# Kernel optimization log

Measured on AMD Instinct MI355X. Metric: run time of the kernel, lower is better.

## Reference

```python
import jax, jax.numpy as jnp
from jax import lax
import numpy as np

K = 3          # kernel_size (must be 3 for shape consistency with the 3x3 sigma conv)
STRIDE = 2
C_IN = 128
EPS = 1e-5     # FrozenBatchNorm2d eps


def setup_inputs() -> dict:
    key = jax.random.key(0)
    k1, k2, k3, k4, k5, k6 = jax.random.split(key, 6)
    x = jax.random.normal(k1, (8, C_IN, 112, 112), dtype=jnp.float32)
    # conv: in_channels -> k*k, 3x3, no bias (kaiming init ~ normal scaled)
    fan_out = K * K * 3 * 3
    conv_w = jax.random.normal(k2, (K * K, C_IN, 3, 3), dtype=jnp.float32) * np.sqrt(2.0 / fan_out)
    bn_w = jax.random.normal(k3, (K * K,), dtype=jnp.float32) * 0.1 + 1.0
    bn_b = jax.random.normal(k4, (K * K,), dtype=jnp.float32) * 0.1
    bn_mean = jax.random.normal(k5, (K * K,), dtype=jnp.float32) * 0.1
    bn_var = jax.random.uniform(k6, (K * K,), dtype=jnp.float32, minval=0.5, maxval=1.5)
    return {"x": x, "conv_w": conv_w, "bn_w": bn_w, "bn_b": bn_b,
            "bn_mean": bn_mean, "bn_var": bn_var}


def _pasa(x, conv_w, bn_w, bn_b, bn_mean, bn_var):
    n, c, h, w = x.shape
    pad = K // 2
    # reflection pad
    xp = jnp.pad(x, ((0, 0), (0, 0), (pad, pad), (pad, pad)), mode="reflect")
    # 3x3 conv, stride 1, VALID on padded input -> same h, w
    sigma = lax.conv_general_dilated(xp, conv_w, (1, 1), "VALID",
                                     dimension_numbers=("NCHW", "OIHW", "NCHW"))
    # frozen BN: affine with fixed running stats
    scale = bn_w / jnp.sqrt(bn_var + EPS)
    shift = bn_b - bn_mean * scale
    sigma = sigma * scale[None, :, None, None] + shift[None, :, None, None]
    sigma = jnp.clip(sigma, 0.0001)                       # clamp min only
    sigma = sigma.reshape(n, 1, K * K, h * w)
    sigma = sigma / jnp.sum(sigma, axis=2, keepdims=True)  # normalize over k*k
    # unfold: k*k shifted views of the padded input (channel-outer, kernel row-major)
    patches = jnp.stack([xp[:, :, i:i + h, j:j + w]
                         for i in range(K) for j in range(K)], axis=2)  # (n,c,9,h,w)
    out = jnp.sum(patches.reshape(n, c, K * K, h * w) * sigma, axis=2).reshape(n, c, h, w)
    return out[:, :, ::STRIDE, ::STRIDE]


def reference(x, conv_w, bn_w, bn_b, bn_mean, bn_var):
    return _pasa(x, conv_w, bn_w, bn_b, bn_mean, bn_var)
```

## Files before the change

### kernel.cpp

```cpp
#include <hip/hip_runtime.h>
#include <hip/hip_bf16.h>

#define NB   8
#define C    128
#define H    112
#define W    112
#define HO   56
#define WO   56
#define KK   9
#define WAVES 16
#define CPW  8
#define WT_ELEMS (C * 3 * 27)

__device__ float g_wt[WT_ELEMS];
__device__ float g_shift[KK];

__global__ void pasa_prep(const float* __restrict__ cw,
                          const float* __restrict__ bw,
                          const float* __restrict__ bb,
                          const float* __restrict__ bm,
                          const float* __restrict__ bv) {
    int idx = blockIdx.x * 256 + threadIdx.x;
    if (idx < WT_ELEMS) {
        int ci = idx / 81;
        int rem = idx % 81;
        int kh = rem / 27;
        int r2 = rem % 27;
        int k  = r2 / 3;
        int kw = r2 % 3;
        float scale = bw[k] / sqrtf(bv[k] + 1e-5f);
        g_wt[idx] = cw[((k * C + ci) * 3 + kh) * 3 + kw] * scale;
    } else if (idx < WT_ELEMS + KK) {
        int k = idx - WT_ELEMS;
        float scale = bw[k] / sqrtf(bv[k] + 1e-5f);
        g_shift[k] = bb[k] - bm[k] * scale;
    }
}

__global__ __launch_bounds__(1024)
void pasa_main(const float* __restrict__ x, float* __restrict__ out) {
    __shared__ float part[WAVES * KK * 64];
    __shared__ float sig[KK * 57];

    const int bid  = blockIdx.x;
    const int n    = bid / HO;
    const int ho   = bid % HO;
    const int tid  = threadIdx.x;
    const int lane = tid & 63;
    const int wv   = __builtin_amdgcn_readfirstlane(tid >> 6);
    const int wo   = lane < WO ? lane : (WO - 1);

    int rows[3];
    rows[0] = (ho == 0) ? 1 : (2 * ho - 1);
    rows[1] = 2 * ho;
    rows[2] = 2 * ho + 1;

    const float* xn = x + (size_t)n * C * H * W;

    float acc[KK];
#pragma unroll
    for (int k = 0; k < KK; ++k) acc[k] = 0.0f;

    for (int i = 0; i < CPW; ++i) {
        const int ci = wv * CPW + i;
        const float* xc = xn + (size_t)ci * (H * W);
        const float* wb = g_wt + ci * 81;
#pragma unroll
        for (int kh = 0; kh < 3; ++kh) {
            const float2 v = *(const float2*)(xc + rows[kh] * W + 2 * wo);
            const float t1 = v.x;
            const float t2 = v.y;
            const float t0 = __shfl_up(t2, 1);
            const float* wr = wb + kh * 27;
#pragma unroll
            for (int k = 0; k < KK; ++k) {
                acc[k] = fmaf(t2, wr[3 * k + 2],
                         fmaf(t1, wr[3 * k + 1],
                         fmaf(t0, wr[3 * k + 0], acc[k])));
            }
        }
    }

#pragma unroll
    for (int k = 0; k < KK; ++k) part[(wv * KK + k) * 64 + lane] = acc[k];
    __syncthreads();

    if (tid < KK * WO) {
        const int k = tid / WO;
        const int w_ = tid % WO;
        float s = 0.0f;
#pragma unroll
        for (int w2 = 0; w2 < WAVES; ++w2) s += part[(w2 * KK + k) * 64 + w_];
        s += g_shift[k];
        s = fmaxf(s, 1e-4f);
        sig[k * 57 + w_] = s;
    }
    __syncthreads();

    float sg[KK];
    float tot = 0.0f;
#pragma unroll
    for (int k = 0; k < KK; ++k) { sg[k] = sig[k * 57 + wo]; tot += sg[k]; }
    const float inv = 1.0f / tot;
#pragma unroll
    for (int k = 0; k < KK; ++k) sg[k] *= inv;

    float* on = out + ((size_t)n * C) * (HO * WO) + ho * WO;
    for (int i = 0; i < CPW; ++i) {
        const int ci = wv * CPW + i;
        const float* xc = xn + (size_t)ci * (H * W);
        float o = 0.0f;
#pragma unroll
        for (int kh = 0; kh < 3; ++kh) {
            const float2 v = *(const float2*)(xc + rows[kh] * W + 2 * wo);
            const float t1 = v.x;
            const float t2 = v.y;
            const float t0 = __shfl_up(t2, 1);
            o = fmaf(t0, sg[kh * 3 + 0],
                fmaf(t1, sg[kh * 3 + 1],
                fmaf(t2, sg[kh * 3 + 2], o)));
        }
        if (lane < WO) on[(size_t)ci * (HO * WO) + lane] = o;
    }
}

extern "C" void kernel_launch(void* const* d_in, const int* in_sizes, int n_in,
                              void* d_out, int out_size, void* d_ws, size_t ws_size,
                              hipStream_t stream) {
    const float* x   = (const float*)d_in[0];
    const float* cw  = (const float*)d_in[1];
    const float* bw  = (const float*)d_in[2];
    const float* bb  = (const float*)d_in[3];
    const float* bm  = (const float*)d_in[4];
    const float* bv  = (const float*)d_in[5];
    float* out = (float*)d_out;

    const int prep_elems = WT_ELEMS + KK;
    pasa_prep<<<(prep_elems + 255) / 256, 256, 0, stream>>>(cw, bw, bb, bm, bv);
    pasa_main<<<NB * HO, 1024, 0, stream>>>(x, out);
}
```

Baseline: 117.9 us.

## Software-pipeline channel row loads and reorder blocks by batch-inner index

```diff
diff --git a/kernel.cpp b/kernel.cpp
--- a/kernel.cpp
+++ b/kernel.cpp
@@ -10,7 +10,7 @@
 #define KK   9
 #define WAVES 16
 #define CPW  8
-#define WT_ELEMS (C * 3 * 27)
+#define WT_ELEMS (C * 81)
 
 __device__ float g_wt[WT_ELEMS];
 __device__ float g_shift[KK];
@@ -37,14 +37,14 @@
     }
 }
 
-__global__ __launch_bounds__(1024)
+__global__ __launch_bounds__(1024, 8)
 void pasa_main(const float* __restrict__ x, float* __restrict__ out) {
     __shared__ float part[WAVES * KK * 64];
     __shared__ float sig[KK * 57];
 
     const int bid  = blockIdx.x;
-    const int n    = bid / HO;
-    const int ho   = bid % HO;
+    const int n    = bid & 7;
+    const int ho   = bid >> 3;
     const int tid  = threadIdx.x;
     const int lane = tid & 63;
     const int wv   = __builtin_amdgcn_readfirstlane(tid >> 6);
@@ -56,28 +56,44 @@
     rows[2] = 2 * ho + 1;
 
     const float* xn = x + (size_t)n * C * H * W;
+    const int ci0 = wv * CPW;
 
     float acc[KK];
 #pragma unroll
     for (int k = 0; k < KK; ++k) acc[k] = 0.0f;
 
-    for (int i = 0; i < CPW; ++i) {
-        const int ci = wv * CPW + i;
+    auto ldrows = [&](int ci, float2* v) {
         const float* xc = xn + (size_t)ci * (H * W);
-        const float* wb = g_wt + ci * 81;
+#pragma unroll
+        for (int kh = 0; kh < 3; ++kh)
+            v[kh] = *(const float2*)(xc + rows[kh] * W + 2 * wo);
+    };
+    auto consume = [&](const float2* v, const float* wb, float* a) {
 #pragma unroll
         for (int kh = 0; kh < 3; ++kh) {
-            const float2 v = *(const float2*)(xc + rows[kh] * W + 2 * wo);
-            const float t1 = v.x;
-            const float t2 = v.y;
+            const float t1 = v[kh].x;
+            const float t2 = v[kh].y;
             const float t0 = __shfl_up(t2, 1);
             const float* wr = wb + kh * 27;
 #pragma unroll
-            for (int k = 0; k < KK; ++k) {
-                acc[k] = fmaf(t2, wr[3 * k + 2],
-                         fmaf(t1, wr[3 * k + 1],
-                         fmaf(t0, wr[3 * k + 0], acc[k])));
-            }
+            for (int k = 0; k < KK; ++k)
+                a[k] = fmaf(t2, wr[3 * k + 2],
+                       fmaf(t1, wr[3 * k + 1],
+                       fmaf(t0, wr[3 * k + 0], a[k])));
+        }
+    };
+
+    {
+        float2 va[3], vb[3];
+        ldrows(ci0 + 0, va);
+        ldrows(ci0 + 1, vb);
+        for (int i = 0; i < CPW; i += 2) {
+            float2 na[3], nb[3];
+            if (i + 2 < CPW) { ldrows(ci0 + i + 2, na); ldrows(ci0 + i + 3, nb); }
+            consume(va, g_wt + (ci0 + i) * 81, acc);
+            consume(vb, g_wt + (ci0 + i + 1) * 81, acc);
+#pragma unroll
+            for (int kh = 0; kh < 3; ++kh) { va[kh] = na[kh]; vb[kh] = nb[kh]; }
         }
     }
 
@@ -106,21 +122,35 @@
     for (int k = 0; k < KK; ++k) sg[k] *= inv;
 
     float* on = out + ((size_t)n * C) * (HO * WO) + ho * WO;
-    for (int i = 0; i < CPW; ++i) {
-        const int ci = wv * CPW + i;
-        const float* xc = xn + (size_t)ci * (H * W);
+    auto apply = [&](const float2* v) {
         float o = 0.0f;
 #pragma unroll
         for (int kh = 0; kh < 3; ++kh) {
-            const float2 v = *(const float2*)(xc + rows[kh] * W + 2 * wo);
-            const float t1 = v.x;
-            const float t2 = v.y;
+            const float t1 = v[kh].x;
+            const float t2 = v[kh].y;
             const float t0 = __shfl_up(t2, 1);
             o = fmaf(t0, sg[kh * 3 + 0],
                 fmaf(t1, sg[kh * 3 + 1],
                 fmaf(t2, sg[kh * 3 + 2], o)));
         }
-        if (lane < WO) on[(size_t)ci * (HO * WO) + lane] = o;
+        return o;
+    };
+    {
+        float2 va[3], vb[3];
+        ldrows(ci0 + 0, va);
+        ldrows(ci0 + 1, vb);
+        for (int i = 0; i < CPW; i += 2) {
+            float2 na[3], nb[3];
+            if (i + 2 < CPW) { ldrows(ci0 + i + 2, na); ldrows(ci0 + i + 3, nb); }
+            const float o0 = apply(va);
+            const float o1 = apply(vb);
+            if (lane < WO) {
+                on[(size_t)(ci0 + i)     * (HO * WO) + lane] = o0;
+                on[(size_t)(ci0 + i + 1) * (HO * WO) + lane] = o1;
+            }
+#pragma unroll
+            for (int kh = 0; kh < 3; ++kh) { va[kh] = na[kh]; vb[kh] = nb[kh]; }
+        }
     }
 }
 
```

Result: no change. 118.1 us (+0.1%).
